# Performance work log

Measured on AMD Instinct MI355X. Metric: run time of the kernel, lower is better.

Reference implementation:

```python
import jax, jax.numpy as jnp
import numpy as np

NHEADS = 16
RANK = 8


def _rope(t):
    # t: (B, H, S, hd); past_len = 0 (no kv cache)
    hd = t.shape[-1]
    S = t.shape[2]
    inv = 1.0 / (10000.0 ** (jnp.arange(0, hd, 2, dtype=jnp.float32) / hd))  # (hd/2,)
    ang = jnp.arange(S, dtype=jnp.float32)[:, None] * inv[None, :]           # (S, hd/2)
    cos = jnp.concatenate([jnp.cos(ang), jnp.cos(ang)], -1)[None, None]      # (1,1,S,hd)
    sin = jnp.concatenate([jnp.sin(ang), jnp.sin(ang)], -1)[None, None]
    t1, t2 = jnp.split(t, 2, axis=-1)
    rot = jnp.concatenate([-t2, t1], -1)
    return t * cos + rot * sin


def _hyper_linear(x, Ws, bs, w1, b1, w2, b2, gA_w, gA_b, gB_w, gB_b):
    # Static path + per-batch dynamic low-rank correction generated from pooled context.
    B, S, D = x.shape
    z = x.mean(axis=1)                              # (B, D) pooled context
    h = jax.nn.silu(z @ w1 + b1)                    # (B, D/ratio)
    c = h @ w2 + b2                                 # (B, dynamic_dim)
    A = (c @ gA_w + gA_b).reshape(B, RANK, D)       # (B, rank, D_in)
    Bm = (c @ gB_w + gB_b).reshape(B, D, RANK)      # (B, D_out, rank)
    xa = jnp.einsum('bsd,brd->bsr', x, A)           # (B, S, rank)
    dyn = jnp.einsum('bsr,bor->bso', xa, Bm) / RANK # (B, S, D_out)
    return x @ Ws + bs + dyn


def _forward(x, Wq, bq, Wo, bo,
             Wk, bk, k_w1, k_b1, k_w2, k_b2, k_gA_w, k_gA_b, k_gB_w, k_gB_b,
             Wv, bv, v_w1, v_b1, v_w2, v_b2, v_gA_w, v_gA_b, v_gB_w, v_gB_b):
    B, S, D = x.shape
    hd = D // NHEADS
    q = x @ Wq + bq
    k = _hyper_linear(x, Wk, bk, k_w1, k_b1, k_w2, k_b2, k_gA_w, k_gA_b, k_gB_w, k_gB_b)
    v = _hyper_linear(x, Wv, bv, v_w1, v_b1, v_w2, v_b2, v_gA_w, v_gA_b, v_gB_w, v_gB_b)
    # (B, S, D) -> (B, H, S, hd)
    q = q.reshape(B, S, NHEADS, hd).transpose(0, 2, 1, 3)
    k = k.reshape(B, S, NHEADS, hd).transpose(0, 2, 1, 3)
    v = v.reshape(B, S, NHEADS, hd).transpose(0, 2, 1, 3)
    q = _rope(q)
    k = _rope(k)
    # causal SDPA (kv_cache is None -> is_causal=True)
    scale = 1.0 / jnp.sqrt(jnp.asarray(hd, dtype=x.dtype))
    scores = jnp.einsum('bhqd,bhkd->bhqk', q, k) * scale
    mask = jnp.tril(jnp.ones((S, S), dtype=bool))
    scores = jnp.where(mask, scores, jnp.asarray(-1e30, dtype=scores.dtype))
    attn = jax.nn.softmax(scores, axis=-1)
    out = jnp.einsum('bhqk,bhkd->bhqd', attn, v)
    out = out.transpose(0, 2, 1, 3).reshape(B, S, D)
    return out @ Wo + bo


def setup_inputs() -> dict:
    key = jax.random.key(0)
    D, HID, DYN = 1024, 256, 64
    B, S = 2, 2048
    ks = jax.random.split(key, 32)
    w = lambda i, shp: jax.random.normal(ks[i], shp, dtype=jnp.float32) * 0.02
    inp = {
        'x': jax.random.normal(ks[0], (B, S, D), dtype=jnp.float32),
        'Wq': w(1, (D, D)), 'bq': jnp.zeros((D,), jnp.float32),
        'Wo': w(2, (D, D)), 'bo': jnp.zeros((D,), jnp.float32),
        'Wk': w(3, (D, D)), 'bk': jnp.zeros((D,), jnp.float32),
        'k_w1': w(4, (D, HID)), 'k_b1': jnp.zeros((HID,), jnp.float32),
        'k_w2': w(5, (HID, DYN)), 'k_b2': jnp.zeros((DYN,), jnp.float32),
        'k_gA_w': w(6, (DYN, RANK * D)), 'k_gA_b': jnp.zeros((RANK * D,), jnp.float32),
        'k_gB_w': w(7, (DYN, D * RANK)), 'k_gB_b': jnp.zeros((D * RANK,), jnp.float32),
        'Wv': w(8, (D, D)), 'bv': jnp.zeros((D,), jnp.float32),
        'v_w1': w(9, (D, HID)), 'v_b1': jnp.zeros((HID,), jnp.float32),
        'v_w2': w(10, (HID, DYN)), 'v_b2': jnp.zeros((DYN,), jnp.float32),
        'v_gA_w': w(11, (DYN, RANK * D)), 'v_gA_b': jnp.zeros((RANK * D,), jnp.float32),
        'v_gB_w': w(12, (DYN, D * RANK)), 'v_gB_b': jnp.zeros((D * RANK,), jnp.float32),
    }
    return inp


def reference(x, Wq, bq, Wo, bo,
              Wk, bk, k_w1, k_b1, k_w2, k_b2, k_gA_w, k_gA_b, k_gB_w, k_gB_b,
              Wv, bv, v_w1, v_b1, v_w2, v_b2, v_gA_w, v_gA_b, v_gB_w, v_gB_b):
    return _forward(x, Wq, bq, Wo, bo,
                    Wk, bk, k_w1, k_b1, k_w2, k_b2, k_gA_w, k_gA_b, k_gB_w, k_gB_b,
                    Wv, bv, v_w1, v_b1, v_w2, v_b2, v_gA_w, v_gA_b, v_gB_w, v_gB_b)
```

## Files before the change

### kernel.cpp

```cpp
#include <hip/hip_runtime.h>
#include <math.h>

#define BB 2
#define SS 2048
#define DD 1024
#define NH 16
#define HDM 64
#define RNK 8

typedef short short8 __attribute__((ext_vector_type(8)));
typedef float floatx4 __attribute__((ext_vector_type(4)));

static __device__ __forceinline__ ushort f2bf(float f) {
  union { float f; unsigned u; } v;
  v.f = f;
  unsigned r = (v.u + 0x7FFFu + ((v.u >> 16) & 1u)) >> 16;
  return (ushort)r;
}
static __device__ __forceinline__ float bf2f(ushort u) {
  union { unsigned u; float f; } v;
  v.u = ((unsigned)u) << 16;
  return v.f;
}
static __device__ __forceinline__ unsigned pack_bf_trunc(float a, float b) {
  union { float f; unsigned u; } x, y;
  x.f = a;
  y.f = b;
  return __builtin_amdgcn_perm(y.u, x.u, 0x07060302u);
}
static __device__ __forceinline__ unsigned pack_bf_rne(float a, float b) {
  union { float f; unsigned u; } x, y;
  x.f = a;
  y.f = b;
  unsigned xu = x.u + 0x7FFFu + ((x.u >> 16) & 1u);
  unsigned yu = y.u + 0x7FFFu + ((y.u >> 16) & 1u);
  return __builtin_amdgcn_perm(yu, xu, 0x07060302u);
}

__global__ __launch_bounds__(256) void z_pool(const float* __restrict__ x,
                                              float* __restrict__ zsum) {
  int b = blockIdx.x;
  int s0 = blockIdx.y * 16;
  int tid = threadIdx.x;
  float p0 = 0.f, p1 = 0.f, p2 = 0.f, p3 = 0.f;
  const float* xp = x + ((size_t)b * SS + s0) * DD;
  for (int s = 0; s < 16; ++s) {
    const float* row = xp + (size_t)s * DD;
    p0 += row[tid];
    p1 += row[tid + 256];
    p2 += row[tid + 512];
    p3 += row[tid + 768];
  }
  atomicAdd(&zsum[b * DD + tid], p0);
  atomicAdd(&zsum[b * DD + tid + 256], p1);
  atomicAdd(&zsum[b * DD + tid + 512], p2);
  atomicAdd(&zsum[b * DD + tid + 768], p3);
}

__global__ __launch_bounds__(256) void gen_h(
    const float* __restrict__ zsum,
    const float* __restrict__ kw1, const float* __restrict__ vw1,
    float* __restrict__ h_pre) {
  int b = blockIdx.x & 1;
  int p = (blockIdx.x >> 1) & 1;
  int slice = blockIdx.y;
  const float* w1 = p ? vw1 : kw1;
  int tid = threadIdx.x;
  float acc = 0.f;
  int j0 = slice * 128;
  for (int j = j0; j < j0 + 128; ++j) {
    float z = zsum[b * DD + j] * (1.0f / (float)SS);
    acc += z * w1[j * 256 + tid];
  }
  atomicAdd(&h_pre[(p * 2 + b) * 256 + tid], acc);
}

__global__ __launch_bounds__(256) void hyper_c2(
    const float* __restrict__ h_pre,
    const float* __restrict__ kb1, const float* __restrict__ kw2,
    const float* __restrict__ kb2,
    const float* __restrict__ vb1, const float* __restrict__ vw2,
    const float* __restrict__ vb2, float* __restrict__ c_all) {
  int p = blockIdx.x >> 1;
  int b = blockIdx.x & 1;
  const float* b1 = p ? vb1 : kb1;
  const float* w2 = p ? vw2 : kw2;
  const float* b2 = p ? vb2 : kb2;
  __shared__ float hs[256];
  __shared__ float part[256];
  int tid = threadIdx.x;
  float hv = h_pre[(p * 2 + b) * 256 + tid] + b1[tid];
  hs[tid] = hv / (1.0f + expf(-hv));
  __syncthreads();
  int n = tid & 63, chunk = tid >> 6;
  float a = 0.f;
  for (int jj = 0; jj < 64; ++jj) {
    int j = chunk * 64 + jj;
    a += hs[j] * w2[j * 64 + n];
  }
  part[tid] = a;
  __syncthreads();
  if (tid < 64) {
    c_all[(p * 2 + b) * 64 + tid] =
        part[tid] + part[tid + 64] + part[tid + 128] + part[tid + 192] + b2[tid];
  }
}

__global__ __launch_bounds__(256) void gen_AB(
    const float* __restrict__ c_all,
    const float* __restrict__ kgAw, const float* __restrict__ kgAb,
    const float* __restrict__ kgBw, const float* __restrict__ kgBb,
    const float* __restrict__ vgAw, const float* __restrict__ vgAb,
    const float* __restrict__ vgBw, const float* __restrict__ vgBb,
    float* __restrict__ Ak, float* __restrict__ Bk,
    float* __restrict__ Av, float* __restrict__ Bv) {
  int y = blockIdx.y;
  int p = y >> 1, mat = y & 1;
  const float* gw = p ? (mat ? vgBw : vgAw) : (mat ? kgBw : kgAw);
  const float* gb = p ? (mat ? vgBb : vgAb) : (mat ? kgBb : kgAb);
  float* obase = p ? (mat ? Bv : Av) : (mat ? Bk : Ak);

  __shared__ float c0[64], c1[64];
  int tid = threadIdx.x;
  if (tid < 64) c0[tid] = c_all[p * 128 + tid];
  else if (tid < 128) c1[tid - 64] = c_all[p * 128 + tid];
  __syncthreads();

  int idx = blockIdx.x * 256 + tid;
  float a0 = gb[idx], a1 = a0;
#pragma unroll
  for (int j = 0; j < 64; ++j) {
    float w = gw[j * (RNK * DD) + idx];
    a0 += c0[j] * w;
    a1 += c1[j] * w;
  }
  obase[idx] = a0;
  obase[RNK * DD + idx] = a1;
}

__global__ __launch_bounds__(256) void cvt_bf16(const float* __restrict__ in,
                                                ushort* __restrict__ out) {
  int gid = blockIdx.x * 256 + threadIdx.x;
  float4 a = ((const float4*)in)[gid];
  ushort4 o;
  o.x = f2bf(a.x);
  o.y = f2bf(a.y);
  o.z = f2bf(a.z);
  o.w = f2bf(a.w);
  ((ushort4*)out)[gid] = o;
}

__global__ __launch_bounds__(256) void cvt_wt(const float* __restrict__ W,
                                              ushort* __restrict__ Wt) {
  __shared__ float tile[32][33];
  int bx = blockIdx.x, by = blockIdx.y;
  int tx = threadIdx.x & 31, ty = threadIdx.x >> 5;
#pragma unroll
  for (int i = 0; i < 4; ++i)
    tile[ty + 8 * i][tx] = W[(size_t)(by * 32 + ty + 8 * i) * DD + bx * 32 + tx];
  __syncthreads();
#pragma unroll
  for (int i = 0; i < 4; ++i)
    Wt[(size_t)(bx * 32 + ty + 8 * i) * DD + by * 32 + tx] =
        f2bf(tile[tx][ty + 8 * i]);
}

__global__ __launch_bounds__(256) void rope_tab(float2* __restrict__ tab) {
  int gid = blockIdx.x * 256 + threadIdx.x;
  int i = gid >> 11, s = gid & 2047;
  float freq = expf(-(float)i * (9.210340371976184f / 32.0f));
  float sn, cn;
  sincosf((float)s * freq, &sn, &cn);
  tab[gid] = make_float2(cn, sn);
}

__global__ __launch_bounds__(256) void weff(
    const float* __restrict__ Ak, const float* __restrict__ Bk,
    const float* __restrict__ Av, const float* __restrict__ Bv,
    const ushort* __restrict__ Wtk, const ushort* __restrict__ Wtv,
    ushort* __restrict__ Wcat) {
  int y = blockIdx.y;
  int p = y >> 1, b = y & 1;
  const float* A = (p ? Av : Ak) + b * (RNK * DD);
  const float* Bm = (p ? Bv : Bk) + b * (RNK * DD);
  const ushort* src = p ? Wtv : Wtk;
  ushort* dst = Wcat + ((size_t)(1 + 2 * p + b) << 20);

  int tid = threadIdx.x;
  int row = blockIdx.x * 16 + (tid >> 4);
  int cg = tid & 15;
  float bm[RNK];
#pragma unroll
  for (int r = 0; r < RNK; ++r) bm[r] = Bm[row * RNK + r];
  for (int kk = cg * 64; kk < cg * 64 + 64; kk += 4) {
    float4 acc = make_float4(0.f, 0.f, 0.f, 0.f);
#pragma unroll
    for (int r = 0; r < RNK; ++r) {
      float4 a4 = *(const float4*)&A[r * DD + kk];
      acc.x += bm[r] * a4.x;
      acc.y += bm[r] * a4.y;
      acc.z += bm[r] * a4.z;
      acc.w += bm[r] * a4.w;
    }
    ushort4 ws = *(const ushort4*)&src[(size_t)row * DD + kk];
    ushort4 o;
    o.x = f2bf(bf2f(ws.x) + acc.x * 0.125f);
    o.y = f2bf(bf2f(ws.y) + acc.y * 0.125f);
    o.z = f2bf(bf2f(ws.z) + acc.z * 0.125f);
    o.w = f2bf(bf2f(ws.w) + acc.w * 0.125f);
    *(ushort4*)&dst[(size_t)row * DD + kk] = o;
  }
}

__global__ __launch_bounds__(256) void gemm_qkv(
    const ushort* __restrict__ Axb, const ushort* __restrict__ Wcat,
    const float* __restrict__ bq, const float* __restrict__ bk,
    const float* __restrict__ bv, const float2* __restrict__ tab,
    ushort* __restrict__ qhb, ushort* __restrict__ khb,
    ushort* __restrict__ vhb) {
  __shared__ ushort As[128][40];
  __shared__ ushort Bs[128][40];
  int tid = threadIdx.x;
  int bm = blockIdx.x * 128;
  int ny = blockIdx.y;
  int path = ny >> 3;
  int nb = (ny & 7) * 128;
  int b_blk = bm >> 11;
  const ushort* Wbase =
      (path == 0) ? Wcat : Wcat + ((size_t)(1 + (path - 1) * 2 + b_blk) << 20);
  const float* bias = (path == 0) ? bq : (path == 1 ? bk : bv);
  ushort* outp = (path == 0) ? qhb : (path == 1 ? khb : vhb);

  int w = tid >> 6, lane = tid & 63, l16 = lane & 15, q4 = lane >> 4;
  int wm = (w >> 1) * 64, wn = (w & 1) * 64;
  floatx4 acc[4][4];
#pragma unroll
  for (int mi = 0; mi < 4; ++mi)
#pragma unroll
    for (int ni = 0; ni < 4; ++ni) acc[mi][ni] = 0;

  int sr = tid >> 2, sc = (tid & 3) * 8;
  const ushort* Ap0 = Axb + (size_t)(bm + sr) * DD + sc;
  const ushort* Ap1 = Axb + (size_t)(bm + sr + 64) * DD + sc;
  const ushort* Bp0 = Wbase + (size_t)(nb + sr) * DD + sc;
  const ushort* Bp1 = Wbase + (size_t)(nb + sr + 64) * DD + sc;

  for (int k0 = 0; k0 < DD; k0 += 32) {
    uint4 a0 = *(const uint4*)(Ap0 + k0);
    uint4 a1 = *(const uint4*)(Ap1 + k0);
    uint4 b0 = *(const uint4*)(Bp0 + k0);
    uint4 b1 = *(const uint4*)(Bp1 + k0);
    __syncthreads();
    *(uint4*)&As[sr][sc] = a0;
    *(uint4*)&As[sr + 64][sc] = a1;
    *(uint4*)&Bs[sr][sc] = b0;
    *(uint4*)&Bs[sr + 64][sc] = b1;
    __syncthreads();
    short8 af[4], bf[4];
#pragma unroll
    for (int mi = 0; mi < 4; ++mi)
      af[mi] = *(const short8*)&As[wm + mi * 16 + l16][q4 * 8];
#pragma unroll
    for (int ni = 0; ni < 4; ++ni)
      bf[ni] = *(const short8*)&Bs[wn + ni * 16 + l16][q4 * 8];
#pragma unroll
    for (int mi = 0; mi < 4; ++mi)
#pragma unroll
      for (int ni = 0; ni < 4; ++ni)
        acc[mi][ni] = __builtin_amdgcn_mfma_f32_16x16x32_bf16(
            af[mi], bf[ni], acc[mi][ni], 0, 0, 0);
  }

  int h = (nb + wn) >> 6;
  float biasv[4];
#pragma unroll
  for (int ni = 0; ni < 4; ++ni) biasv[ni] = bias[nb + wn + ni * 16 + l16];

#pragma unroll
  for (int mi = 0; mi < 4; ++mi) {
#pragma unroll
    for (int r = 0; r < 4; ++r) {
      int grow = bm + wm + mi * 16 + q4 * 4 + r;
      int bb = grow >> 11, s = grow & 2047;
      ushort* orow = outp + (((size_t)(bb * NH + h) * SS + s) << 6);
      float v[4];
#pragma unroll
      for (int ni = 0; ni < 4; ++ni) v[ni] = acc[mi][ni][r] + biasv[ni];
      if (path < 2) {
#pragma unroll
        for (int ni = 0; ni < 2; ++ni) {
          float2 cs = tab[((ni * 16 + l16) << 11) + s];
          float a = v[ni] * cs.x - v[ni + 2] * cs.y;
          float c = v[ni + 2] * cs.x + v[ni] * cs.y;
          v[ni] = a;
          v[ni + 2] = c;
        }
      }
#pragma unroll
      for (int ni = 0; ni < 4; ++ni) orow[ni * 16 + l16] = f2bf(v[ni]);
    }
  }
}

#define VT_IDX(d, c) ((unsigned)(72 * (d) + 16 * ((d) >> 3) + (c)))

__global__ __launch_bounds__(128) void attn_mfma3(
    const ushort* __restrict__ qh, const ushort* __restrict__ kh,
    const ushort* __restrict__ vh, ushort* __restrict__ ao) {
  __shared__ ushort Ps[64][72];
  __shared__ ushort Vt[2][4720];
  int bid = blockIdx.x;
  int bh = bid & 31;
  int q0 = (31 - (bid >> 5)) * 64;
  int b = bh >> 4, h = bh & 15;
  int tid = threadIdx.x;
  int w = tid >> 6, lane = tid & 63, l16 = lane & 15, q4 = lane >> 4;
  int nkt = (q0 >> 6) + 1;

  const ushort* kbase = kh + (size_t)bh * SS * HDM;
  const ushort* vbase = vh + (size_t)bh * SS * HDM;

  short8 qf[2][2];
#pragma unroll
  for (int qi = 0; qi < 2; ++qi) {
    const ushort* qrow = qh + ((size_t)bh * SS + q0 + 32 * w + 16 * qi + l16) * HDM;
    qf[qi][0] = *(const short8*)(qrow + 8 * q4);
    qf[qi][1] = *(const short8*)(qrow + 32 + 8 * q4);
  }

  int so8 = tid & 7, sp = (tid >> 3) & 15;

  short8 kf[4][2];
#pragma unroll
  for (int ki = 0; ki < 4; ++ki) {
    const ushort* kr = kbase + (size_t)(16 * ki + l16) * HDM + 8 * q4;
    kf[ki][0] = *(const short8*)(kr);
    kf[ki][1] = *(const short8*)(kr + 32);
  }
  uint4 vr[4];
#pragma unroll
  for (int j = 0; j < 4; ++j)
    vr[j] = *(const uint4*)(vbase + (size_t)(4 * sp + j) * HDM + 8 * so8);
#pragma unroll
  for (int j = 0; j < 4; j += 2) {
    const ushort* pa = (const ushort*)&vr[j];
    const ushort* pb = (const ushort*)&vr[j + 1];
#pragma unroll
    for (int dd = 0; dd < 8; ++dd) {
      int d = so8 * 8 + dd;
      *(unsigned*)&Vt[0][VT_IDX(d, 4 * sp + j)] =
          (unsigned)pa[dd] | ((unsigned)pb[dd] << 16);
    }
  }
  __syncthreads();

  floatx4 o[4][2];
#pragma unroll
  for (int di = 0; di < 4; ++di)
#pragma unroll
    for (int qi = 0; qi < 2; ++qi) o[di][qi] = 0;
  float l_part[2] = {0.f, 0.f};

  for (int kt = 0; kt < nkt; ++kt) {
    int buf = kt & 1;
    bool has_next = (kt + 1) < nkt;
    short8 kn[4][2];
    if (has_next) {
      int k0n = (kt + 1) * 64;
#pragma unroll
      for (int ki = 0; ki < 4; ++ki) {
        const ushort* kr = kbase + (size_t)(k0n + 16 * ki + l16) * HDM + 8 * q4;
        kn[ki][0] = *(const short8*)(kr);
        kn[ki][1] = *(const short8*)(kr + 32);
      }
#pragma unroll
      for (int j = 0; j < 4; ++j)
        vr[j] = *(const uint4*)(vbase + (size_t)(k0n + 4 * sp + j) * HDM + 8 * so8);
    }

    floatx4 s4[2][4];
#pragma unroll
    for (int ki = 0; ki < 4; ++ki)
#pragma unroll
      for (int qi = 0; qi < 2; ++qi) {
        floatx4 c;
        c = 0;
        c = __builtin_amdgcn_mfma_f32_16x16x32_bf16(kf[ki][0], qf[qi][0], c, 0, 0, 0);
        c = __builtin_amdgcn_mfma_f32_16x16x32_bf16(kf[ki][1], qf[qi][1], c, 0, 0, 0);
        s4[qi][ki] = c;
      }

    bool diag = (kt == nkt - 1);
#pragma unroll
    for (int qi = 0; qi < 2; ++qi) {
      int qloc = 32 * w + 16 * qi + l16;
      float lp = 0.f;
#pragma unroll
      for (int ki = 0; ki < 4; ++ki) {
        float p[4];
#pragma unroll
        for (int r = 0; r < 4; ++r) {
          float t = s4[qi][ki][r] * 0.18033688f;
          float pv = exp2f(t);
          if (diag && (16 * ki + 4 * q4 + r) > qloc) pv = 0.f;
          p[r] = pv;
          lp += pv;
        }
        unsigned u0 = pack_bf_trunc(p[0], p[1]);
        unsigned u1 = pack_bf_trunc(p[2], p[3]);
        uint2 u2;
        u2.x = u0;
        u2.y = u1;
        *(uint2*)&Ps[qloc][16 * ki + 4 * q4] = u2;
      }
      l_part[qi] += lp;
    }

#pragma unroll
    for (int qi = 0; qi < 2; ++qi) {
      short8 pf0 = *(const short8*)&Ps[32 * w + 16 * qi + l16][8 * q4];
      short8 pf1 = *(const short8*)&Ps[32 * w + 16 * qi + l16][32 + 8 * q4];
#pragma unroll
      for (int di = 0; di < 4; ++di) {
        short8 vf0 = *(const short8*)&Vt[buf][VT_IDX(16 * di + l16, 8 * q4)];
        short8 vf1 = *(const short8*)&Vt[buf][VT_IDX(16 * di + l16, 32 + 8 * q4)];
        o[di][qi] =
            __builtin_amdgcn_mfma_f32_16x16x32_bf16(vf0, pf0, o[di][qi], 0, 0, 0);
        o[di][qi] =
            __builtin_amdgcn_mfma_f32_16x16x32_bf16(vf1, pf1, o[di][qi], 0, 0, 0);
      }
    }

    if (has_next) {
      int nb = (kt + 1) & 1;
#pragma unroll
      for (int j = 0; j < 4; j += 2) {
        const ushort* pa = (const ushort*)&vr[j];
        const ushort* pb = (const ushort*)&vr[j + 1];
#pragma unroll
        for (int dd = 0; dd < 8; ++dd) {
          int d = so8 * 8 + dd;
          *(unsigned*)&Vt[nb][VT_IDX(d, 4 * sp + j)] =
              (unsigned)pa[dd] | ((unsigned)pb[dd] << 16);
        }
      }
#pragma unroll
      for (int ki = 0; ki < 4; ++ki) {
        kf[ki][0] = kn[ki][0];
        kf[ki][1] = kn[ki][1];
      }
    }
    __syncthreads();
  }

#pragma unroll
  for (int qi = 0; qi < 2; ++qi) {
    float l = l_part[qi];
    l += __shfl_xor(l, 16);
    l += __shfl_xor(l, 32);
    float inv = 1.0f / l;
    int token = q0 + 32 * w + 16 * qi + l16;
    ushort* orow = ao + ((size_t)(b * SS + token)) * DD + h * HDM;
#pragma unroll
    for (int di = 0; di < 4; ++di) {
      floatx4 ov = o[di][qi];
      uint2 u2;
      u2.x = pack_bf_rne(ov[0] * inv, ov[1] * inv);
      u2.y = pack_bf_rne(ov[2] * inv, ov[3] * inv);
      *(uint2*)&orow[16 * di + 4 * q4] = u2;
    }
  }
}

__global__ __launch_bounds__(256) void gemm_out(
    const ushort* __restrict__ A, const ushort* __restrict__ Bt,
    const float* __restrict__ bias, float* __restrict__ C) {
  __shared__ ushort As[64][40];
  __shared__ ushort Bs[128][40];
  int tid = threadIdx.x;
  int bm = blockIdx.x * 64, bn = blockIdx.y * 128;
  int w = tid >> 6, lane = tid & 63, l16 = lane & 15, q4 = lane >> 4;
  int wm = (w >> 1) * 32, wn = (w & 1) * 64;
  floatx4 acc[2][4];
#pragma unroll
  for (int mi = 0; mi < 2; ++mi)
#pragma unroll
    for (int ni = 0; ni < 4; ++ni) acc[mi][ni] = 0;

  int sr = tid >> 2, sc = (tid & 3) * 8;
  const ushort* Ap0 = A + (size_t)(bm + sr) * DD + sc;
  const ushort* Bp0 = Bt + (size_t)(bn + sr) * DD + sc;
  const ushort* Bp1 = Bt + (size_t)(bn + sr + 64) * DD + sc;

  for (int k0 = 0; k0 < DD; k0 += 32) {
    uint4 a0 = *(const uint4*)(Ap0 + k0);
    uint4 b0 = *(const uint4*)(Bp0 + k0);
    uint4 b1 = *(const uint4*)(Bp1 + k0);
    __syncthreads();
    *(uint4*)&As[sr & 63][sc] = a0;
    *(uint4*)&Bs[sr][sc] = b0;
    *(uint4*)&Bs[sr + 64][sc] = b1;
    __syncthreads();
    short8 af[2], bf[4];
#pragma unroll
    for (int mi = 0; mi < 2; ++mi)
      af[mi] = *(const short8*)&As[wm + mi * 16 + l16][q4 * 8];
#pragma unroll
    for (int ni = 0; ni < 4; ++ni)
      bf[ni] = *(const short8*)&Bs[wn + ni * 16 + l16][q4 * 8];
#pragma unroll
    for (int mi = 0; mi < 2; ++mi)
#pragma unroll
      for (int ni = 0; ni < 4; ++ni)
        acc[mi][ni] = __builtin_amdgcn_mfma_f32_16x16x32_bf16(
            af[mi], bf[ni], acc[mi][ni], 0, 0, 0);
  }
#pragma unroll
  for (int mi = 0; mi < 2; ++mi) {
#pragma unroll
    for (int r = 0; r < 4; ++r) {
      int row = bm + wm + mi * 16 + q4 * 4 + r;
      float* Cr = C + (size_t)row * DD;
#pragma unroll
      for (int ni = 0; ni < 4; ++ni) {
        int col = bn + wn + ni * 16 + l16;
        Cr[col] = acc[mi][ni][r] + bias[col];
      }
    }
  }
}

extern "C" void kernel_launch(void* const* d_in, const int* in_sizes, int n_in,
                              void* d_out, int out_size, void* d_ws,
                              size_t ws_size, hipStream_t stream) {
  const float* x    = (const float*)d_in[0];
  const float* Wq   = (const float*)d_in[1];
  const float* bq   = (const float*)d_in[2];
  const float* Wo   = (const float*)d_in[3];
  const float* bo   = (const float*)d_in[4];
  const float* Wk   = (const float*)d_in[5];
  const float* bk   = (const float*)d_in[6];
  const float* kw1  = (const float*)d_in[7];
  const float* kb1  = (const float*)d_in[8];
  const float* kw2  = (const float*)d_in[9];
  const float* kb2  = (const float*)d_in[10];
  const float* kgAw = (const float*)d_in[11];
  const float* kgAb = (const float*)d_in[12];
  const float* kgBw = (const float*)d_in[13];
  const float* kgBb = (const float*)d_in[14];
  const float* Wv   = (const float*)d_in[15];
  const float* bv   = (const float*)d_in[16];
  const float* vw1  = (const float*)d_in[17];
  const float* vb1  = (const float*)d_in[18];
  const float* vw2  = (const float*)d_in[19];
  const float* vb2  = (const float*)d_in[20];
  const float* vgAw = (const float*)d_in[21];
  const float* vgAb = (const float*)d_in[22];
  const float* vgBw = (const float*)d_in[23];
  const float* vgBb = (const float*)d_in[24];
  float* out = (float*)d_out;

  char* ws = (char*)d_ws;
  const size_t MB = 1024 * 1024;
  ushort* qhb  = (ushort*)(ws);
  ushort* khb  = (ushort*)(ws + 8 * MB);
  ushort* vhb  = (ushort*)(ws + 16 * MB);
  ushort* xb   = (ushort*)(ws + 24 * MB);
  ushort* aob  = (ushort*)(ws + 32 * MB);
  ushort* Wcat = (ushort*)(ws + 40 * MB);
  ushort* Wto  = (ushort*)(ws + 50 * MB);
  ushort* Wtk  = (ushort*)(ws + 52 * MB);
  ushort* Wtv  = (ushort*)(ws + 54 * MB);
  float*  Ak   = (float*)(ws + 56 * MB);
  float*  Bk   = Ak + BB * RNK * DD;
  float*  Av   = Bk + BB * RNK * DD;
  float*  Bv   = Av + BB * RNK * DD;
  float*  zsum = Bv + BB * RNK * DD;
  float*  h_pre = zsum + BB * DD;
  float*  c_all = h_pre + 4 * 256;
  float2* tab  = (float2*)(ws + 56 * MB + 512 * 1024);

  hipMemsetAsync(zsum, 0, (BB * DD + 4 * 256) * sizeof(float), stream);
  z_pool<<<dim3(BB, SS / 16), 256, 0, stream>>>(x, zsum);
  gen_h<<<dim3(4, 8), 256, 0, stream>>>(zsum, kw1, vw1, h_pre);
  hyper_c2<<<4, 256, 0, stream>>>(h_pre, kb1, kw2, kb2, vb1, vw2, vb2, c_all);
  gen_AB<<<dim3(RNK * DD / 256, 4), 256, 0, stream>>>(
      c_all, kgAw, kgAb, kgBw, kgBb, vgAw, vgAb, vgBw, vgBb, Ak, Bk, Av, Bv);

  cvt_bf16<<<(BB * SS * DD / 4) / 256, 256, 0, stream>>>(x, xb);
  cvt_wt<<<dim3(32, 32), 256, 0, stream>>>(Wq, Wcat);
  cvt_wt<<<dim3(32, 32), 256, 0, stream>>>(Wk, Wtk);
  cvt_wt<<<dim3(32, 32), 256, 0, stream>>>(Wv, Wtv);
  cvt_wt<<<dim3(32, 32), 256, 0, stream>>>(Wo, Wto);
  rope_tab<<<(32 * 2048) / 256, 256, 0, stream>>>(tab);
  weff<<<dim3(64, 4), 256, 0, stream>>>(Ak, Bk, Av, Bv, Wtk, Wtv, Wcat);

  gemm_qkv<<<dim3(32, 24), 256, 0, stream>>>(xb, Wcat, bq, bk, bv, tab, qhb,
                                             khb, vhb);
  attn_mfma3<<<1024, 128, 0, stream>>>(qhb, khb, vhb, aob);
  gemm_out<<<dim3(64, 8), 256, 0, stream>>>(aob, Wto, bo, out);
}
```

Baseline: 325.0 us.

## Split attention KV tiles across wave pairs with private smem and final reduction

The attention kernel goes from 128 to 256 threads. Two wave pairs each handle alternate KV tiles for the same 64 queries, using per-wave private V-transpose and P buffers, so the per-tile __syncthreads is gone. Partial outputs and row sums are combined through shared memory at the end. This doubles the waves working on each query block and removes barrier stalls, at the cost of extra shared memory, a reduction step, and one redundant prefetch per wave at loop exit.

```diff
diff --git a/kernel.cpp b/kernel.cpp
--- a/kernel.cpp
+++ b/kernel.cpp
@@ -304,55 +304,51 @@
 
 #define VT_IDX(d, c) ((unsigned)(72 * (d) + 16 * ((d) >> 3) + (c)))
 
-__global__ __launch_bounds__(128) void attn_mfma3(
-    const ushort* __restrict__ qh, const ushort* __restrict__ kh,
-    const ushort* __restrict__ vh, ushort* __restrict__ ao) {
-  __shared__ ushort Ps[64][72];
-  __shared__ ushort Vt[2][4720];
+__global__ __launch_bounds__(256) void attn_mfma4(
+    const ushort* __restrict__ qhp, const ushort* __restrict__ khp,
+    const ushort* __restrict__ vhp, ushort* __restrict__ ao) {
+  __shared__ ushort smem[28096];
   int bid = blockIdx.x;
   int bh = bid & 31;
   int q0 = (31 - (bid >> 5)) * 64;
   int b = bh >> 4, h = bh & 15;
   int tid = threadIdx.x;
   int w = tid >> 6, lane = tid & 63, l16 = lane & 15, q4 = lane >> 4;
+  int qhl = w & 1, kc = w >> 1;
   int nkt = (q0 >> 6) + 1;
 
-  const ushort* kbase = kh + (size_t)bh * SS * HDM;
-  const ushort* vbase = vh + (size_t)bh * SS * HDM;
+  ushort* Vt = smem + w * 4720;
+  ushort* Ps = smem + 18880 + w * 2304;
+
+  const ushort* kbase = khp + (size_t)bh * SS * HDM;
+  const ushort* vbase = vhp + (size_t)bh * SS * HDM;
 
   short8 qf[2][2];
 #pragma unroll
   for (int qi = 0; qi < 2; ++qi) {
-    const ushort* qrow = qh + ((size_t)bh * SS + q0 + 32 * w + 16 * qi + l16) * HDM;
+    const ushort* qrow =
+        qhp + ((size_t)bh * SS + q0 + 32 * qhl + 16 * qi + l16) * HDM;
     qf[qi][0] = *(const short8*)(qrow + 8 * q4);
     qf[qi][1] = *(const short8*)(qrow + 32 + 8 * q4);
   }
 
-  int so8 = tid & 7, sp = (tid >> 3) & 15;
+  int so8 = lane & 7, sp = lane >> 3;
 
   short8 kf[4][2];
-#pragma unroll
-  for (int ki = 0; ki < 4; ++ki) {
-    const ushort* kr = kbase + (size_t)(16 * ki + l16) * HDM + 8 * q4;
-    kf[ki][0] = *(const short8*)(kr);
-    kf[ki][1] = *(const short8*)(kr + 32);
-  }
-  uint4 vr[4];
-#pragma unroll
-  for (int j = 0; j < 4; ++j)
-    vr[j] = *(const uint4*)(vbase + (size_t)(4 * sp + j) * HDM + 8 * so8);
-#pragma unroll
-  for (int j = 0; j < 4; j += 2) {
-    const ushort* pa = (const ushort*)&vr[j];
-    const ushort* pb = (const ushort*)&vr[j + 1];
-#pragma unroll
-    for (int dd = 0; dd < 8; ++dd) {
-      int d = so8 * 8 + dd;
-      *(unsigned*)&Vt[0][VT_IDX(d, 4 * sp + j)] =
-          (unsigned)pa[dd] | ((unsigned)pb[dd] << 16);
-    }
-  }
-  __syncthreads();
+  uint4 vr[8];
+  {
+    int k0 = kc * 64;
+#pragma unroll
+    for (int ki = 0; ki < 4; ++ki) {
+      const ushort* kr = kbase + (size_t)(k0 + 16 * ki + l16) * HDM + 8 * q4;
+      kf[ki][0] = *(const short8*)(kr);
+      kf[ki][1] = *(const short8*)(kr + 32);
+    }
+#pragma unroll
+    for (int j = 0; j < 8; ++j)
+      vr[j] =
+          *(const uint4*)(vbase + (size_t)(k0 + 8 * sp + j) * HDM + 8 * so8);
+  }
 
   floatx4 o[4][2];
 #pragma unroll
@@ -361,96 +357,83 @@
     for (int qi = 0; qi < 2; ++qi) o[di][qi] = 0;
   float l_part[2] = {0.f, 0.f};
 
-  for (int kt = 0; kt < nkt; ++kt) {
-    int buf = kt & 1;
-    bool has_next = (kt + 1) < nkt;
-    short8 kn[4][2];
-    if (has_next) {
-      int k0n = (kt + 1) * 64;
+  for (int kt = kc; kt < nkt; kt += 2) {
+#pragma unroll
+    for (int jj = 0; jj < 8; jj += 2) {
+      const ushort* pa = (const ushort*)&vr[jj];
+      const ushort* pb = (const ushort*)&vr[jj + 1];
+#pragma unroll
+      for (int dd = 0; dd < 8; ++dd)
+        *(unsigned*)&Vt[VT_IDX(8 * so8 + dd, 8 * sp + jj)] =
+            (unsigned)pa[dd] | ((unsigned)pb[dd] << 16);
+    }
+    bool diag = (kt == nkt - 1);
+#pragma unroll
+    for (int qi = 0; qi < 2; ++qi) {
+      floatx4 s4[4];
 #pragma unroll
       for (int ki = 0; ki < 4; ++ki) {
-        const ushort* kr = kbase + (size_t)(k0n + 16 * ki + l16) * HDM + 8 * q4;
-        kn[ki][0] = *(const short8*)(kr);
-        kn[ki][1] = *(const short8*)(kr + 32);
-      }
-#pragma unroll
-      for (int j = 0; j < 4; ++j)
-        vr[j] = *(const uint4*)(vbase + (size_t)(k0n + 4 * sp + j) * HDM + 8 * so8);
-    }
-
-    floatx4 s4[2][4];
-#pragma unroll
-    for (int ki = 0; ki < 4; ++ki)
-#pragma unroll
-      for (int qi = 0; qi < 2; ++qi) {
         floatx4 c;
         c = 0;
-        c = __builtin_amdgcn_mfma_f32_16x16x32_bf16(kf[ki][0], qf[qi][0], c, 0, 0, 0);
-        c = __builtin_amdgcn_mfma_f32_16x16x32_bf16(kf[ki][1], qf[qi][1], c, 0, 0, 0);
-        s4[qi][ki] = c;
+        c = __builtin_amdgcn_mfma_f32_16x16x32_bf16(kf[ki][0], qf[qi][0], c, 0,
+                                                    0, 0);
+        c = __builtin_amdgcn_mfma_f32_16x16x32_bf16(kf[ki][1], qf[qi][1], c, 0,
+                                                    0, 0);
+        s4[ki] = c;
       }
-
-    bool diag = (kt == nkt - 1);
-#pragma unroll
-    for (int qi = 0; qi < 2; ++qi) {
-      int qloc = 32 * w + 16 * qi + l16;
+      int qloc = 32 * qhl + 16 * qi + l16;
       float lp = 0.f;
 #pragma unroll
       for (int ki = 0; ki < 4; ++ki) {
         float p[4];
 #pragma unroll
         for (int r = 0; r < 4; ++r) {
-          float t = s4[qi][ki][r] * 0.18033688f;
+          float t = s4[ki][r] * 0.18033688f;
           float pv = exp2f(t);
           if (diag && (16 * ki + 4 * q4 + r) > qloc) pv = 0.f;
           p[r] = pv;
           lp += pv;
         }
-        unsigned u0 = pack_bf_trunc(p[0], p[1]);
-        unsigned u1 = pack_bf_trunc(p[2], p[3]);
         uint2 u2;
-        u2.x = u0;
-        u2.y = u1;
-        *(uint2*)&Ps[qloc][16 * ki + 4 * q4] = u2;
+        u2.x = pack_bf_trunc(p[0], p[1]);
+        u2.y = pack_bf_trunc(p[2], p[3]);
+        *(uint2*)&Ps[(16 * qi + l16) * 72 + 16 * ki + 4 * q4] = u2;
       }
       l_part[qi] += lp;
     }
-
+    {
+      int kp = kt + 2;
+      int k0n = (kp < nkt ? kp : 0) * 64;
+#pragma unroll
+      for (int ki = 0; ki < 4; ++ki) {
+        const ushort* kr =
+            kbase + (size_t)(k0n + 16 * ki + l16) * HDM + 8 * q4;
+        kf[ki][0] = *(const short8*)(kr);
+        kf[ki][1] = *(const short8*)(kr + 32);
+      }
+#pragma unroll
+      for (int j = 0; j < 8; ++j)
+        vr[j] =
+            *(const uint4*)(vbase + (size_t)(k0n + 8 * sp + j) * HDM + 8 * so8);
+    }
+    short8 pf[2][2];
 #pragma unroll
     for (int qi = 0; qi < 2; ++qi) {
-      short8 pf0 = *(const short8*)&Ps[32 * w + 16 * qi + l16][8 * q4];
-      short8 pf1 = *(const short8*)&Ps[32 * w + 16 * qi + l16][32 + 8 * q4];
-#pragma unroll
-      for (int di = 0; di < 4; ++di) {
-        short8 vf0 = *(const short8*)&Vt[buf][VT_IDX(16 * di + l16, 8 * q4)];
-        short8 vf1 = *(const short8*)&Vt[buf][VT_IDX(16 * di + l16, 32 + 8 * q4)];
-        o[di][qi] =
-            __builtin_amdgcn_mfma_f32_16x16x32_bf16(vf0, pf0, o[di][qi], 0, 0, 0);
-        o[di][qi] =
-            __builtin_amdgcn_mfma_f32_16x16x32_bf16(vf1, pf1, o[di][qi], 0, 0, 0);
+      pf[qi][0] = *(const short8*)&Ps[(16 * qi + l16) * 72 + 8 * q4];
+      pf[qi][1] = *(const short8*)&Ps[(16 * qi + l16) * 72 + 32 + 8 * q4];
+    }
+#pragma unroll
+    for (int di = 0; di < 4; ++di) {
+      short8 vf0 = *(const short8*)&Vt[VT_IDX(16 * di + l16, 8 * q4)];
+      short8 vf1 = *(const short8*)&Vt[VT_IDX(16 * di + l16, 32 + 8 * q4)];
+#pragma unroll
+      for (int qi = 0; qi < 2; ++qi) {
+        o[di][qi] = __builtin_amdgcn_mfma_f32_16x16x32_bf16(vf0, pf[qi][0],
+                                                            o[di][qi], 0, 0, 0);
+        o[di][qi] = __builtin_amdgcn_mfma_f32_16x16x32_bf16(vf1, pf[qi][1],
+                                                            o[di][qi], 0, 0, 0);
       }
     }
-
-    if (has_next) {
-      int nb = (kt + 1) & 1;
-#pragma unroll
-      for (int j = 0; j < 4; j += 2) {
-        const ushort* pa = (const ushort*)&vr[j];
-        const ushort* pb = (const ushort*)&vr[j + 1];
-#pragma unroll
-        for (int dd = 0; dd < 8; ++dd) {
-          int d = so8 * 8 + dd;
-          *(unsigned*)&Vt[nb][VT_IDX(d, 4 * sp + j)] =
-              (unsigned)pa[dd] | ((unsigned)pb[dd] << 16);
-        }
-      }
-#pragma unroll
-      for (int ki = 0; ki < 4; ++ki) {
-        kf[ki][0] = kn[ki][0];
-        kf[ki][1] = kn[ki][1];
-      }
-    }
-    __syncthreads();
   }
 
 #pragma unroll
@@ -458,15 +441,45 @@
     float l = l_part[qi];
     l += __shfl_xor(l, 16);
     l += __shfl_xor(l, 32);
-    float inv = 1.0f / l;
-    int token = q0 + 32 * w + 16 * qi + l16;
-    ushort* orow = ao + ((size_t)(b * SS + token)) * DD + h * HDM;
-#pragma unroll
-    for (int di = 0; di < 4; ++di) {
-      floatx4 ov = o[di][qi];
+    l_part[qi] = l;
+  }
+
+  __syncthreads();
+  float4* stg = (float4*)smem;
+  float* Ls = (float*)((char*)smem + 32768);
+#pragma unroll
+  for (int di = 0; di < 4; ++di)
+#pragma unroll
+    for (int qi = 0; qi < 2; ++qi) {
+      float4 f;
+      f.x = o[di][qi][0];
+      f.y = o[di][qi][1];
+      f.z = o[di][qi][2];
+      f.w = o[di][qi][3];
+      stg[(w * 8 + di * 2 + qi) * 64 + lane] = f;
+    }
+  if (q4 == 0) {
+#pragma unroll
+    for (int qi = 0; qi < 2; ++qi)
+      Ls[kc * 64 + 32 * qhl + 16 * qi + l16] = l_part[qi];
+  }
+  __syncthreads();
+
+#pragma unroll
+  for (int dii = 0; dii < 2; ++dii) {
+    int di = kc * 2 + dii;
+#pragma unroll
+    for (int qi = 0; qi < 2; ++qi) {
+      float4 fA = stg[(qhl * 8 + di * 2 + qi) * 64 + lane];
+      float4 fB = stg[((2 + qhl) * 8 + di * 2 + qi) * 64 + lane];
+      int q = 32 * qhl + 16 * qi + l16;
+      float ltot = Ls[q] + Ls[64 + q];
+      float inv = 1.0f / ltot;
+      int token = q0 + q;
+      ushort* orow = ao + ((size_t)(b * SS + token)) * DD + h * HDM;
       uint2 u2;
-      u2.x = pack_bf_rne(ov[0] * inv, ov[1] * inv);
-      u2.y = pack_bf_rne(ov[2] * inv, ov[3] * inv);
+      u2.x = pack_bf_rne((fA.x + fB.x) * inv, (fA.y + fB.y) * inv);
+      u2.y = pack_bf_rne((fA.z + fB.z) * inv, (fA.w + fB.w) * inv);
       *(uint2*)&orow[16 * di + 4 * q4] = u2;
     }
   }
@@ -597,6 +610,6 @@
 
   gemm_qkv<<<dim3(32, 24), 256, 0, stream>>>(xb, Wcat, bq, bk, bv, tab, qhb,
                                              khb, vhb);
-  attn_mfma3<<<1024, 128, 0, stream>>>(qhb, khb, vhb, aob);
+  attn_mfma4<<<1024, 256, 0, stream>>>(qhb, khb, vhb, aob);
   gemm_out<<<dim3(64, 8), 256, 0, stream>>>(aob, Wto, bo, out);
 }
```

After: 395.1 us. +21.6%, slower.
